# Kernel optimization log

Measured on AMD Instinct MI355X. Metric: run time of the kernel, lower is better.

Reference implementation:

```python
import jax, jax.numpy as jnp
import numpy as np

B, T, D = 2, 2048, 2048
H, DH, DR, DL = 16, 128, 64, 512
WINDOW, STRIDE, GLOBAL = 512, 64, 128
BASE, MAX_SEQ, ORIG_MAX = 10000.0, 131072, 4096
BETA_FAST, BETA_SLOW = 32.0, 1.0
SCALE = 1.0 / np.sqrt(DH)
SCALE_ROPE = 1.0 / np.sqrt(DR)


def _yarn_inv_freq():
    base_inv = 1.0 / (BASE ** (np.arange(0, DR, 2, dtype=np.float32) / DR))
    scale = MAX_SEQ / ORIG_MAX
    freqs = np.arange(DR // 2, dtype=np.float32)
    ramp = np.clip((freqs - BETA_SLOW) / (BETA_FAST - BETA_SLOW), 0.0, 1.0)
    return jnp.asarray(base_inv * (1 - ramp) + (base_inv / scale) * ramp)

_INV_FREQ = _yarn_inv_freq()
_YARN_FACTOR = np.float32(0.1 * np.log(MAX_SEQ / ORIG_MAX) + 1.0)


def _apply_rope(x):
    # x: [B, H, T, DR]
    t = jnp.arange(x.shape[2], dtype=jnp.float32)
    fr = t[:, None] * _INV_FREQ[None, :]            # [T, DR/2]
    emb = jnp.concatenate([fr, fr], axis=-1)        # [T, DR]
    cos, sin = jnp.cos(emb), jnp.sin(emb)
    x1, x2 = jnp.split(x, 2, axis=-1)
    rot = jnp.concatenate([-x2, x1], axis=-1)
    return (x * cos + rot * sin) * _YARN_FACTOR


def _sparse_mask(seq_len):
    pos = jnp.arange(seq_len)
    qp, kp = pos[:, None], pos[None, :]
    dist = qp - kp
    half = WINDOW // 2
    window = (dist >= -half) & (dist <= half)
    dilated = (kp % STRIDE == 0) | (kp < GLOBAL)
    causal = kp <= qp
    return (window | dilated) & causal              # [T, T] bool


def setup_inputs() -> dict:
    key = jax.random.key(0)
    ks = jax.random.split(key, 9)
    s = 0.02
    return {
        "x": jax.random.normal(ks[0], (B, T, D), jnp.float32),
        "w_q": jax.random.normal(ks[1], (D, D), jnp.float32) * s,
        "w_dkv": jax.random.normal(ks[2], (D, DL), jnp.float32) * s,
        "w_uk": jax.random.normal(ks[3], (DL, D), jnp.float32) * s,
        "w_uv": jax.random.normal(ks[4], (DL, D), jnp.float32) * s,
        "w_q_pos": jax.random.normal(ks[5], (D, H * DR), jnp.float32) * s,
        "w_k_pos": jax.random.normal(ks[6], (D, H * DR), jnp.float32) * s,
        "w_o": jax.random.normal(ks[7], (D, D), jnp.float32) * s,
    }


def reference(x, w_q, w_dkv, w_uk, w_uv, w_q_pos, w_k_pos, w_o):
    b, t, _ = x.shape
    # MLA projections
    q_c = (x @ w_q).reshape(b, t, H, DH).transpose(0, 2, 1, 3)      # [B,H,T,DH]
    c_kv = x @ w_dkv                                                # [B,T,DL]
    k_c = (c_kv @ w_uk).reshape(b, t, H, DH).transpose(0, 2, 1, 3)
    v_c = (c_kv @ w_uv).reshape(b, t, H, DH).transpose(0, 2, 1, 3)
    # decoupled RoPE branch (YaRN)
    q_r = (x @ w_q_pos).reshape(b, t, H, DR).transpose(0, 2, 1, 3)
    k_r = (x @ w_k_pos).reshape(b, t, H, DR).transpose(0, 2, 1, 3)
    q_r = _apply_rope(q_r)
    k_r = _apply_rope(k_r)
    # combined content + positional scores
    scores = jnp.einsum("bhqd,bhkd->bhqk", q_c, k_c) * SCALE \
           + jnp.einsum("bhqr,bhkr->bhqk", q_r, k_r) * SCALE_ROPE
    mask = _sparse_mask(t)                                          # [T,T]
    scores = jnp.where(mask[None, None], scores, -jnp.inf)
    attn = jax.nn.softmax(scores, axis=-1)
    out = jnp.einsum("bhqk,bhkd->bhqd", attn, v_c)                  # [B,H,T,DH]
    out = out.transpose(0, 2, 1, 3).reshape(b, t, D)
    return out @ w_o
```

## Files before the change

kernel.cpp:

```cpp
#include <hip/hip_runtime.h>
#include <hip/hip_bf16.h>
#include <cstdint>

typedef __attribute__((ext_vector_type(8))) short short8_t;
typedef __attribute__((ext_vector_type(4))) short short4_t;
typedef __attribute__((ext_vector_type(4))) float f32x4_t;

#define AS1 __attribute__((address_space(1)))
#define AS3 __attribute__((address_space(3)))

__device__ __forceinline__ void gload_lds16(const void* g, void* l) {
  __builtin_amdgcn_global_load_lds((const AS1 void*)g, (AS3 void*)l, 16, 0, 0);
}

__device__ __forceinline__ short8_t ld8(const __hip_bfloat16* p) {
  return *(const short8_t*)p;
}

__global__ __launch_bounds__(256) void k_prep(
    const float* __restrict__ x, __hip_bfloat16* __restrict__ xb,
    const float* __restrict__ wq,  const float* __restrict__ wqp,
    const float* __restrict__ wkp, const float* __restrict__ wdkv,
    const float* __restrict__ wuk, const float* __restrict__ wuv,
    const float* __restrict__ wo,
    __hip_bfloat16* __restrict__ Bt1, __hip_bfloat16* __restrict__ Bt2,
    __hip_bfloat16* __restrict__ woT) {
  __shared__ float t[64][65];
  int bid = blockIdx.x;
  if (bid < 4096) {
    int i = (bid * 256 + threadIdx.x) * 8;
    union { short8_t v; __hip_bfloat16 h[8]; } u;
#pragma unroll
    for (int j = 0; j < 8; ++j) u.h[j] = __float2bfloat16(x[i + j]);
    *(short8_t*)(xb + i) = u.v;
    return;
  }
  bid -= 4096;
  const float* in; __hip_bfloat16* out; int R, C, tile;
  if (bid < 1024)      { in = wq;   out = Bt1;                 R = 2048; C = 2048; tile = bid; }
  else if (bid < 1536) { in = wqp;  out = Bt1 + 2048UL * 2048; R = 2048; C = 1024; tile = bid - 1024; }
  else if (bid < 2048) { in = wkp;  out = Bt1 + 3072UL * 2048; R = 2048; C = 1024; tile = bid - 1536; }
  else if (bid < 2304) { in = wdkv; out = Bt1 + 4096UL * 2048; R = 2048; C = 512;  tile = bid - 2048; }
  else if (bid < 2560) { in = wuk;  out = Bt2;                 R = 512;  C = 2048; tile = bid - 2304; }
  else if (bid < 2816) { in = wuv;  out = Bt2 + 2048UL * 512;  R = 512;  C = 2048; tile = bid - 2560; }
  else                 { in = wo;   out = woT;                 R = 2048; C = 2048; tile = bid - 2816; }
  int nct = C >> 6;
  int ct = tile % nct, rt = tile / nct;
  int r0 = rt << 6, c0 = ct << 6;
#pragma unroll
  for (int i = 0; i < 16; ++i) {
    int idx = i * 256 + threadIdx.x;
    int r = idx >> 6, c = idx & 63;
    t[r][c] = in[(size_t)(r0 + r) * C + c0 + c];
  }
  __syncthreads();
#pragma unroll
  for (int i = 0; i < 16; ++i) {
    int idx = i * 256 + threadIdx.x;
    int c = idx >> 6, r = idx & 63;
    out[(size_t)(c0 + c) * R + r0 + r] = __float2bfloat16(t[r][c]);
  }
}

template<int MODE>
__global__ __launch_bounds__(256) void k_gemm2(const __hip_bfloat16* __restrict__ A,
                                               const __hip_bfloat16* __restrict__ Bt,
                                               int K, int nbx,
                                               void* __restrict__ O0, float alpha) {
  __shared__ __align__(16) __hip_bfloat16 Al[3][128 * 32];
  __shared__ __align__(16) __hip_bfloat16 Bl[3][128 * 32];
  int bx = blockIdx.x % nbx, by = blockIdx.x / nbx;
  int tid = threadIdx.x, lane = tid & 63, w = tid >> 6;
  int L = lane & 15, hi = lane >> 4;
  int wr = (w >> 1) << 6, wc = (w & 1) << 6;
  f32x4_t acc[4][4] = {};
  const __hip_bfloat16* Ag = A + (size_t)(by * 128) * K;
  const __hip_bfloat16* Bg = Bt + (size_t)(bx * 128) * K;
  int rA = w * 16 + (lane >> 2);
  int cA = ((lane & 3) ^ ((lane >> 3) & 3)) * 8;
  int NT = K >> 5;

  auto stage = [&](int s) {
    int j = s % 3;
    int k0 = s << 5;
    gload_lds16(Ag + (size_t)rA * K + k0 + cA,        &Al[j][(w * 16) * 32]);
    gload_lds16(Ag + (size_t)(rA + 64) * K + k0 + cA, &Al[j][(64 + w * 16) * 32]);
    gload_lds16(Bg + (size_t)rA * K + k0 + cA,        &Bl[j][(w * 16) * 32]);
    gload_lds16(Bg + (size_t)(rA + 64) * K + k0 + cA, &Bl[j][(64 + w * 16) * 32]);
  };

  stage(0); stage(1);
  asm volatile("s_waitcnt vmcnt(4)\ns_barrier" ::: "memory");

  int hs = hi ^ ((L >> 1) & 3);
  for (int t = 0; t < NT; ++t) {
    int j = t % 3;
    short8_t af[4], bf[4];
#pragma unroll
    for (int m = 0; m < 4; ++m) af[m] = ld8(&Al[j][(wr + 16 * m + L) * 32 + 8 * hs]);
#pragma unroll
    for (int n = 0; n < 4; ++n) bf[n] = ld8(&Bl[j][(wc + 16 * n + L) * 32 + 8 * hs]);
    if (t + 2 < NT) stage(t + 2);
    __builtin_amdgcn_s_setprio(1);
#pragma unroll
    for (int m = 0; m < 4; ++m)
#pragma unroll
      for (int n = 0; n < 4; ++n)
        acc[m][n] = __builtin_amdgcn_mfma_f32_16x16x32_bf16(af[m], bf[n], acc[m][n], 0, 0, 0);
    __builtin_amdgcn_s_setprio(0);
    if (t + 2 < NT)      asm volatile("s_waitcnt vmcnt(4)\ns_barrier" ::: "memory");
    else if (t + 1 < NT) asm volatile("s_waitcnt vmcnt(0)\ns_barrier" ::: "memory");
  }

  int r0 = by * 128 + wr + 4 * hi;
  int c0 = bx * 128 + wc;
  size_t N = (size_t)nbx << 7;
  float* C = (float*)O0;
#pragma unroll
  for (int m = 0; m < 4; ++m)
#pragma unroll
    for (int n = 0; n < 4; ++n)
#pragma unroll
      for (int i = 0; i < 4; ++i)
        C[(size_t)(r0 + 16 * m + i) * N + c0 + 16 * n + L] = acc[m][n][i] * alpha;
}

__global__ __launch_bounds__(256) void k_gemm_ks(const __hip_bfloat16* __restrict__ A,
                                                 const __hip_bfloat16* __restrict__ Bt,
                                                 int lda, int nbx,
                                                 float* __restrict__ P0,
                                                 float* __restrict__ P1) {
  __shared__ __align__(16) __hip_bfloat16 Al[3][128 * 32];
  __shared__ __align__(16) __hip_bfloat16 Bl[3][128 * 32];
  int part = blockIdx.x >> 7;
  int id = blockIdx.x & 127;
  int bx = id % nbx, by = id / nbx;
  int tid = threadIdx.x, lane = tid & 63, w = tid >> 6;
  int L = lane & 15, hi = lane >> 4;
  int wr = (w >> 1) << 6, wc = (w & 1) << 6;
  f32x4_t acc[4][4] = {};
  const __hip_bfloat16* Ag = A + (size_t)(by * 128) * lda + part * 1024;
  const __hip_bfloat16* Bg = Bt + (size_t)(bx * 128) * lda + part * 1024;
  int rA = w * 16 + (lane >> 2);
  int cA = ((lane & 3) ^ ((lane >> 3) & 3)) * 8;
  const int NT = 32;

  auto stage = [&](int s) {
    int j = s % 3;
    int k0 = s << 5;
    gload_lds16(Ag + (size_t)rA * lda + k0 + cA,        &Al[j][(w * 16) * 32]);
    gload_lds16(Ag + (size_t)(rA + 64) * lda + k0 + cA, &Al[j][(64 + w * 16) * 32]);
    gload_lds16(Bg + (size_t)rA * lda + k0 + cA,        &Bl[j][(w * 16) * 32]);
    gload_lds16(Bg + (size_t)(rA + 64) * lda + k0 + cA, &Bl[j][(64 + w * 16) * 32]);
  };

  stage(0); stage(1);
  asm volatile("s_waitcnt vmcnt(4)\ns_barrier" ::: "memory");

  int hs = hi ^ ((L >> 1) & 3);
  for (int t = 0; t < NT; ++t) {
    int j = t % 3;
    short8_t af[4], bf[4];
#pragma unroll
    for (int m = 0; m < 4; ++m) af[m] = ld8(&Al[j][(wr + 16 * m + L) * 32 + 8 * hs]);
#pragma unroll
    for (int n = 0; n < 4; ++n) bf[n] = ld8(&Bl[j][(wc + 16 * n + L) * 32 + 8 * hs]);
    if (t + 2 < NT) stage(t + 2);
    __builtin_amdgcn_s_setprio(1);
#pragma unroll
    for (int m = 0; m < 4; ++m)
#pragma unroll
      for (int n = 0; n < 4; ++n)
        acc[m][n] = __builtin_amdgcn_mfma_f32_16x16x32_bf16(af[m], bf[n], acc[m][n], 0, 0, 0);
    __builtin_amdgcn_s_setprio(0);
    if (t + 2 < NT)      asm volatile("s_waitcnt vmcnt(4)\ns_barrier" ::: "memory");
    else if (t + 1 < NT) asm volatile("s_waitcnt vmcnt(0)\ns_barrier" ::: "memory");
  }

  float* C = part ? P1 : P0;
  int r0 = by * 128 + wr + 4 * hi;
  int c0 = bx * 128 + wc;
#pragma unroll
  for (int m = 0; m < 4; ++m)
#pragma unroll
    for (int n = 0; n < 4; ++n)
#pragma unroll
      for (int i = 0; i < 4; ++i)
        C[(size_t)(r0 + 16 * m + i) * 512 + c0 + 16 * n + L] = acc[m][n][i];
}

__global__ __launch_bounds__(256) void k_addc(const float* __restrict__ P0,
                                              const float* __restrict__ P1,
                                              __hip_bfloat16* __restrict__ ckv) {
  int i = (blockIdx.x * 256 + threadIdx.x) * 4;
  float4 a = *(const float4*)(P0 + i);
  float4 b = *(const float4*)(P1 + i);
  union { short4_t v; __hip_bfloat16 h[4]; } u;
  u.h[0] = __float2bfloat16(a.x + b.x);
  u.h[1] = __float2bfloat16(a.y + b.y);
  u.h[2] = __float2bfloat16(a.z + b.z);
  u.h[3] = __float2bfloat16(a.w + b.w);
  *(short4_t*)(ckv + i) = u.v;
}

template<int MODE>
__global__ __launch_bounds__(512, 2) void k_gemm8(const __hip_bfloat16* __restrict__ A,
                                                  const __hip_bfloat16* __restrict__ Bt,
                                                  int K, int nbx,
                                                  void* __restrict__ O0, void* __restrict__ O1,
                                                  void* __restrict__ O2) {
  __shared__ __align__(16) __hip_bfloat16 Al[3][256 * 32];
  __shared__ __align__(16) __hip_bfloat16 Bl[3][256 * 32];
  int bx = blockIdx.x % nbx, by = blockIdx.x / nbx;
  int tid = threadIdx.x, lane = tid & 63, w = tid >> 6;
  int L = lane & 15, hi = lane >> 4;
  int wr = (w >> 2) << 7;
  int wc = (w & 3) << 6;
  f32x4_t acc[8][4] = {};
  const __hip_bfloat16* Ag = A + (size_t)(by * 256) * K;
  const __hip_bfloat16* Bg = Bt + (size_t)(bx * 256) * K;
  int rA = w * 16 + (lane >> 2);
  int cA = ((lane & 3) ^ ((lane >> 3) & 3)) * 8;
  int NT = K >> 5;

  auto stage = [&](int s) {
    int j = s % 3;
    int k0 = s << 5;
    gload_lds16(Ag + (size_t)rA * K + k0 + cA,         &Al[j][(w * 16) * 32]);
    gload_lds16(Ag + (size_t)(rA + 128) * K + k0 + cA, &Al[j][(128 + w * 16) * 32]);
    gload_lds16(Bg + (size_t)rA * K + k0 + cA,         &Bl[j][(w * 16) * 32]);
    gload_lds16(Bg + (size_t)(rA + 128) * K + k0 + cA, &Bl[j][(128 + w * 16) * 32]);
  };

  stage(0); stage(1);
  asm volatile("s_waitcnt vmcnt(4)\ns_barrier" ::: "memory");

  int hs = hi ^ ((L >> 1) & 3);
  for (int t = 0; t < NT; ++t) {
    int j = t % 3;
    short8_t af[8], bf[4];
#pragma unroll
    for (int m = 0; m < 8; ++m) af[m] = ld8(&Al[j][(wr + 16 * m + L) * 32 + 8 * hs]);
#pragma unroll
    for (int n = 0; n < 4; ++n) bf[n] = ld8(&Bl[j][(wc + 16 * n + L) * 32 + 8 * hs]);
    if (t + 2 < NT) stage(t + 2);
    __builtin_amdgcn_s_setprio(1);
#pragma unroll
    for (int m = 0; m < 8; ++m)
#pragma unroll
      for (int n = 0; n < 4; ++n)
        acc[m][n] = __builtin_amdgcn_mfma_f32_16x16x32_bf16(af[m], bf[n], acc[m][n], 0, 0, 0);
    __builtin_amdgcn_s_setprio(0);
    if (t + 2 < NT)      asm volatile("s_waitcnt vmcnt(4)\ns_barrier" ::: "memory");
    else if (t + 1 < NT) asm volatile("s_waitcnt vmcnt(0)\ns_barrier" ::: "memory");
  }

  int r0 = by * 256 + wr + 4 * hi;
  int cb = bx * 256 + wc;

  if (MODE == 2) {
    __hip_bfloat16* qcb = (__hip_bfloat16*)O0;
    __hip_bfloat16* qrb = (__hip_bfloat16*)O1;
    __hip_bfloat16* krb = (__hip_bfloat16*)O2;
    if (cb < 2048) {
      const float SCALE = 0.08838834764831845f;
#pragma unroll
      for (int m = 0; m < 8; ++m)
#pragma unroll
        for (int n = 0; n < 4; ++n)
#pragma unroll
          for (int i = 0; i < 4; ++i)
            qcb[(size_t)(r0 + 16 * m + i) * 2048 + cb + 16 * n + L] =
                __float2bfloat16(acc[m][n][i] * SCALE);
    } else {
      bool isq = cb < 3072;
      __hip_bfloat16* dst = isq ? qrb : krb;
      float osc = isq ? 0.16832169878499666f : 1.3465735902799727f;
      int cbl = cb - (isq ? 2048 : 3072);
      float invf[2];
#pragma unroll
      for (int p = 0; p < 2; ++p) {
        float fi = (float)(16 * p + L);
        float bi = __expf(fi * -0.28782313662425574f);
        float ramp = fminf(fmaxf((fi - 1.0f) * (1.0f / 31.0f), 0.0f), 1.0f);
        invf[p] = bi * (1.0f - ramp * (31.0f / 32.0f));
      }
#pragma unroll
      for (int m = 0; m < 8; ++m)
#pragma unroll
        for (int i = 0; i < 4; ++i) {
          int row = r0 + 16 * m + i;
          float ft = (float)(row & 2047);
#pragma unroll
          for (int p = 0; p < 2; ++p) {
            float sn, cs;
            __sincosf(ft * invf[p], &sn, &cs);
            float x1 = acc[m][p][i], x2 = acc[m][p + 2][i];
            dst[(size_t)row * 1024 + cbl + 16 * p + L] =
                __float2bfloat16((x1 * cs - x2 * sn) * osc);
            dst[(size_t)row * 1024 + cbl + 32 + 16 * p + L] =
                __float2bfloat16((x2 * cs + x1 * sn) * osc);
          }
        }
    }
  } else if (MODE == 3) {
    __hip_bfloat16* kcb = (__hip_bfloat16*)O0;
    __hip_bfloat16* vcb = (__hip_bfloat16*)O1;
    __hip_bfloat16* vT  = (__hip_bfloat16*)O2;
    if (cb < 2048) {
#pragma unroll
      for (int m = 0; m < 8; ++m)
#pragma unroll
        for (int n = 0; n < 4; ++n)
#pragma unroll
          for (int i = 0; i < 4; ++i)
            kcb[(size_t)(r0 + 16 * m + i) * 2048 + cb + 16 * n + L] =
                __float2bfloat16(acc[m][n][i]);
    } else {
#pragma unroll
      for (int m = 0; m < 8; ++m)
#pragma unroll
        for (int n = 0; n < 4; ++n) {
          int vcol = cb - 2048 + 16 * n + L;
          int hh = vcol >> 7, dh = vcol & 127;
          int row0 = r0 + 16 * m;
          int b = row0 >> 11, t0 = row0 & 2047;
          union { short4_t v; __hip_bfloat16 h4[4]; } pk;
#pragma unroll
          for (int i = 0; i < 4; ++i) {
            __hip_bfloat16 bv = __float2bfloat16(acc[m][n][i]);
            vcb[(size_t)(row0 + i) * 2048 + vcol] = bv;
            pk.h4[i] = bv;
          }
          *(short4_t*)(vT + ((size_t)((b * 16 + hh) * 128 + dh) * 2048 + t0)) = pk.v;
        }
    }
  }
}

__global__ __launch_bounds__(256) void k_attn(const __hip_bfloat16* __restrict__ qc,
                                              const __hip_bfloat16* __restrict__ kc,
                                              const __hip_bfloat16* __restrict__ vcb,
                                              const __hip_bfloat16* __restrict__ qr,
                                              const __hip_bfloat16* __restrict__ kr,
                                              const __hip_bfloat16* __restrict__ vT,
                                              __hip_bfloat16* __restrict__ ao) {
  const int T = 2048;
  int bid = blockIdx.x;
  int qt = 31 - (bid >> 5);
  int bh = bid & 31;
  int b = bh >> 4, h = bh & 15;
  int tid = threadIdx.x, lane = tid & 63, w = tid >> 6;
  int L = lane & 15, hi = lane >> 4;
  int q0 = qt * 64;

  __shared__ __align__(16) __hip_bfloat16 Kl[64 * 192];
  __shared__ __align__(16) __hip_bfloat16 Vt[128 * 64];
  __shared__ __align__(16) __hip_bfloat16 Pl[4][16 * 64];
  char* Klb = (char*)Kl;
  char* Vtb = (char*)Vt;
  char* Plb = (char*)Pl;

  const __hip_bfloat16* vTb = vT + (size_t)(b * 16 + h) * 128 * 2048;

  int qrow = q0 + w * 16 + L;
  size_t qb = (size_t)b * T + qrow;
  short8_t qf[6];
#pragma unroll
  for (int c = 0; c < 4; ++c)
    qf[c] = ld8(qc + qb * 2048 + h * 128 + 32 * c + 8 * hi);
#pragma unroll
  for (int c = 0; c < 2; ++c)
    qf[4 + c] = ld8(qr + qb * 1024 + h * 64 + 32 * c + 8 * hi);

  f32x4_t oacc[8] = {};
  float lpart[4] = {0.0f, 0.0f, 0.0f, 0.0f};

  int nd = qt - 6;

  for (int step = 0; step <= qt + 1; ++step) {
    bool compact = (step == qt + 1);
    if (compact && nd <= 0) break;
    int kt = step;
    if (!compact && kt > 1 && kt < qt - 4) continue;
    int k0 = kt * 64;

#pragma unroll
    for (int i = 0; i < 6; ++i) {
      int o = i * 256 + tid;
      int rr = o / 24;
      int cs = o % 24;
      int c = cs ^ (rr & 7);
      int d = c * 8;
      int srcr = compact ? ((rr < nd) ? 64 * (2 + rr) : 0) : (k0 + rr);
      size_t krow = (size_t)b * T + srcr;
      const __hip_bfloat16* src = (d < 128)
          ? kc + krow * 2048 + h * 128 + d
          : kr + krow * 1024 + h * 64 + (d - 128);
      gload_lds16(src, Klb + (i * 256 + w * 64) * 16);
    }
    if (!compact) {
#pragma unroll
      for (int i = 0; i < 4; ++i) {
        int o = i * 256 + tid;
        int row = o >> 3, cs = o & 7;
        int c = cs ^ (row & 7);
        gload_lds16(vTb + (size_t)row * 2048 + k0 + c * 8,
                    Vtb + (i * 256 + w * 64) * 16);
      }
    } else {
#pragma unroll
      for (int i = 0; i < 2; ++i) {
        int ch = i * 256 + tid;
        int jj = ch >> 4, d0 = (ch & 15) * 8;
        if (jj < nd) {
          union { short8_t v; __hip_bfloat16 hh[8]; } u;
          u.v = ld8(vcb + (size_t)(b * 2048 + 64 * (2 + jj)) * 2048 + h * 128 + d0);
#pragma unroll
          for (int qq = 0; qq < 8; ++qq) {
            int dh = d0 + qq;
            int swc = (jj >> 3) ^ (dh & 7);
            *(__hip_bfloat16*)(Vtb + dh * 128 + 16 * swc + 2 * (jj & 7)) = u.hh[qq];
          }
        }
      }
    }
    __syncthreads();

    f32x4_t sacc[4] = {};
    __builtin_amdgcn_s_setprio(1);
#pragma unroll
    for (int n = 0; n < 4; ++n) {
      int row = 16 * n + L;
#pragma unroll
      for (int c = 0; c < 6; ++c) {
        short8_t bfr = *(const short8_t*)(Klb + row * 384 + 16 * ((4 * c + hi) ^ (row & 7)));
        sacc[n] = __builtin_amdgcn_mfma_f32_16x16x32_bf16(qf[c], bfr, sacc[n], 0, 0, 0);
      }
    }
    __builtin_amdgcn_s_setprio(0);

    int rbase = q0 + w * 16 + 4 * hi;
#pragma unroll
    for (int n = 0; n < 4; ++n) {
      int col = L + 16 * n;
      int k = k0 + col;
#pragma unroll
      for (int i = 0; i < 4; ++i) {
        int rq = rbase + i;
        bool ok = compact ? (col < nd)
                          : ((k <= rq) && ((rq - k <= 256) || ((k & 63) == 0) || (k < 128)));
        float e = ok ? __expf(sacc[n][i]) : 0.0f;
        lpart[i] += e;
        int row = 4 * hi + i;
        int cc = (2 * n + (L >> 3)) ^ (row & 7);
        *(__hip_bfloat16*)(Plb + w * 2048 + row * 128 + 16 * cc + 2 * (L & 7)) =
            __float2bfloat16(e);
      }
    }

    __builtin_amdgcn_s_setprio(1);
#pragma unroll
    for (int ks = 0; ks < 2; ++ks) {
      short8_t pa = *(const short8_t*)(Plb + w * 2048 + L * 128 +
                                       16 * ((4 * ks + hi) ^ (L & 7)));
#pragma unroll
      for (int n = 0; n < 8; ++n) {
        int vrow = 16 * n + L;
        int chunk = (4 * ks + hi) ^ (vrow & 7);
        short8_t bv = *(const short8_t*)(Vtb + vrow * 128 + 16 * chunk);
        oacc[n] = __builtin_amdgcn_mfma_f32_16x16x32_bf16(pa, bv, oacc[n], 0, 0, 0);
      }
    }
    __builtin_amdgcn_s_setprio(0);
    __syncthreads();
  }

  for (int d = 1; d < 16; d <<= 1)
#pragma unroll
    for (int i = 0; i < 4; ++i) lpart[i] += __shfl_xor(lpart[i], d, 64);

#pragma unroll
  for (int n = 0; n < 8; ++n)
#pragma unroll
    for (int i = 0; i < 4; ++i) {
      int rq = q0 + w * 16 + 4 * hi + i;
      int cdh = 16 * n + L;
      float v = oacc[n][i] / lpart[i];
      ao[((size_t)b * T + rq) * 2048 + h * 128 + cdh] = __float2bfloat16(v);
    }
}

extern "C" void kernel_launch(void* const* d_in, const int* in_sizes, int n_in,
                              void* d_out, int out_size, void* d_ws, size_t ws_size,
                              hipStream_t stream) {
  const float* x     = (const float*)d_in[0];
  const float* w_q   = (const float*)d_in[1];
  const float* w_dkv = (const float*)d_in[2];
  const float* w_uk  = (const float*)d_in[3];
  const float* w_uv  = (const float*)d_in[4];
  const float* w_qp  = (const float*)d_in[5];
  const float* w_kp  = (const float*)d_in[6];
  const float* w_o   = (const float*)d_in[7];
  float* out = (float*)d_out;

  char* ws = (char*)d_ws;
  size_t off = 0;
  auto alloc = [&](size_t elems) {
    __hip_bfloat16* p = (__hip_bfloat16*)(ws + off);
    off += ((elems * 2 + 255) & ~(size_t)255);
    return p;
  };
  __hip_bfloat16* xb  = alloc(8388608);
  __hip_bfloat16* Bt1 = alloc(4608UL * 2048);
  __hip_bfloat16* Bt2 = alloc(4096UL * 512);
  __hip_bfloat16* woT = alloc(4194304);
  __hip_bfloat16* qcb = alloc(8388608);
  __hip_bfloat16* ckv = alloc(2097152);
  __hip_bfloat16* kcb = alloc(8388608);
  __hip_bfloat16* vcb = alloc(8388608);
  __hip_bfloat16* qrb = alloc(4194304);
  __hip_bfloat16* krb = alloc(4194304);
  __hip_bfloat16* aob = alloc(8388608);
  __hip_bfloat16* vT  = alloc(8388608);

  float* P0 = (float*)aob;
  float* P1 = P0 + 2097152;

  k_prep<<<7936, 256, 0, stream>>>(x, xb, w_q, w_qp, w_kp, w_dkv, w_uk, w_uv, w_o,
                                   Bt1, Bt2, woT);

  k_gemm_ks<<<256, 256, 0, stream>>>(xb, Bt1 + 4096UL * 2048, 2048, 4, P0, P1);
  k_addc<<<2048, 256, 0, stream>>>(P0, P1, ckv);

  k_gemm8<2><<<16 * 16, 512, 0, stream>>>(xb, Bt1, 2048, 16, qcb, qrb, krb);
  k_gemm8<3><<<16 * 16, 512, 0, stream>>>(ckv, Bt2, 512, 16, kcb, vcb, vT);

  k_attn<<<1024, 256, 0, stream>>>(qcb, kcb, vcb, qrb, krb, vT, aob);

  k_gemm2<1><<<16 * 32, 256, 0, stream>>>(aob, woT, 2048, 16, out, 1.0f);
}
```

Baseline: 244.8 us.

## Switch gemm to double-buffered BK=64 tiles with XOR-swizzled LDS layout

Replaces the 3-stage, BK=32 LDS pipeline in the bf16 GEMM with a 2-stage pipeline using BK=64 tiles. Each tile now goes through an 8-way XOR swizzle on 16-byte chunks. It halves the number of barriers and K-loop iterations and widens each global-to-LDS load batch. In exchange it prefetches only one tile ahead, waits on vmcnt(0) every iteration, and uses more LDS: 128 KB instead of 96 KB, which may limit the two blocks per CU that the launch bounds ask for.

```diff
diff --git a/kernel.cpp b/kernel.cpp
--- a/kernel.cpp
+++ b/kernel.cpp
@@ -209,8 +209,8 @@
                                                   int K, int nbx,
                                                   void* __restrict__ O0, void* __restrict__ O1,
                                                   void* __restrict__ O2) {
-  __shared__ __align__(16) __hip_bfloat16 Al[3][256 * 32];
-  __shared__ __align__(16) __hip_bfloat16 Bl[3][256 * 32];
+  __shared__ __align__(16) __hip_bfloat16 Al[2][256 * 64];
+  __shared__ __align__(16) __hip_bfloat16 Bl[2][256 * 64];
   int bx = blockIdx.x % nbx, by = blockIdx.x / nbx;
   int tid = threadIdx.x, lane = tid & 63, w = tid >> 6;
   int L = lane & 15, hi = lane >> 4;
@@ -219,40 +219,55 @@
   f32x4_t acc[8][4] = {};
   const __hip_bfloat16* Ag = A + (size_t)(by * 256) * K;
   const __hip_bfloat16* Bg = Bt + (size_t)(bx * 256) * K;
-  int rA = w * 16 + (lane >> 2);
-  int cA = ((lane & 3) ^ ((lane >> 3) & 3)) * 8;
-  int NT = K >> 5;
+  int NT = K >> 6;
 
   auto stage = [&](int s) {
-    int j = s % 3;
-    int k0 = s << 5;
-    gload_lds16(Ag + (size_t)rA * K + k0 + cA,         &Al[j][(w * 16) * 32]);
-    gload_lds16(Ag + (size_t)(rA + 128) * K + k0 + cA, &Al[j][(128 + w * 16) * 32]);
-    gload_lds16(Bg + (size_t)rA * K + k0 + cA,         &Bl[j][(w * 16) * 32]);
-    gload_lds16(Bg + (size_t)(rA + 128) * K + k0 + cA, &Bl[j][(128 + w * 16) * 32]);
+    int j = s & 1;
+    int k0 = s << 6;
+#pragma unroll
+    for (int i = 0; i < 4; ++i) {
+      int o = i * 512 + tid;
+      int rr = o >> 3, cs = o & 7;
+      int c = cs ^ (rr & 7);
+      gload_lds16(Ag + (size_t)rr * K + k0 + c * 8, (char*)Al[j] + (size_t)o * 16);
+    }
+#pragma unroll
+    for (int i = 0; i < 4; ++i) {
+      int o = i * 512 + tid;
+      int rr = o >> 3, cs = o & 7;
+      int c = cs ^ (rr & 7);
+      gload_lds16(Bg + (size_t)rr * K + k0 + c * 8, (char*)Bl[j] + (size_t)o * 16);
+    }
   };
 
-  stage(0); stage(1);
-  asm volatile("s_waitcnt vmcnt(4)\ns_barrier" ::: "memory");
-
-  int hs = hi ^ ((L >> 1) & 3);
+  stage(0);
+  asm volatile("s_waitcnt vmcnt(0)\ns_barrier" ::: "memory");
+
   for (int t = 0; t < NT; ++t) {
-    int j = t % 3;
-    short8_t af[8], bf[4];
-#pragma unroll
-    for (int m = 0; m < 8; ++m) af[m] = ld8(&Al[j][(wr + 16 * m + L) * 32 + 8 * hs]);
-#pragma unroll
-    for (int n = 0; n < 4; ++n) bf[n] = ld8(&Bl[j][(wc + 16 * n + L) * 32 + 8 * hs]);
-    if (t + 2 < NT) stage(t + 2);
-    __builtin_amdgcn_s_setprio(1);
-#pragma unroll
-    for (int m = 0; m < 8; ++m)
-#pragma unroll
-      for (int n = 0; n < 4; ++n)
-        acc[m][n] = __builtin_amdgcn_mfma_f32_16x16x32_bf16(af[m], bf[n], acc[m][n], 0, 0, 0);
-    __builtin_amdgcn_s_setprio(0);
-    if (t + 2 < NT)      asm volatile("s_waitcnt vmcnt(4)\ns_barrier" ::: "memory");
-    else if (t + 1 < NT) asm volatile("s_waitcnt vmcnt(0)\ns_barrier" ::: "memory");
+    int j = t & 1;
+    if (t + 1 < NT) stage(t + 1);
+#pragma unroll
+    for (int sub = 0; sub < 2; ++sub) {
+      short8_t af[8], bf[4];
+#pragma unroll
+      for (int m = 0; m < 8; ++m) {
+        int row = wr + 16 * m + L;
+        af[m] = *(const short8_t*)((char*)Al[j] + row * 128 + 16 * ((4 * sub + hi) ^ (row & 7)));
+      }
+#pragma unroll
+      for (int n = 0; n < 4; ++n) {
+        int row = wc + 16 * n + L;
+        bf[n] = *(const short8_t*)((char*)Bl[j] + row * 128 + 16 * ((4 * sub + hi) ^ (row & 7)));
+      }
+      __builtin_amdgcn_s_setprio(1);
+#pragma unroll
+      for (int m = 0; m < 8; ++m)
+#pragma unroll
+        for (int n = 0; n < 4; ++n)
+          acc[m][n] = __builtin_amdgcn_mfma_f32_16x16x32_bf16(af[m], bf[n], acc[m][n], 0, 0, 0);
+      __builtin_amdgcn_s_setprio(0);
+    }
+    if (t + 1 < NT) asm volatile("s_waitcnt vmcnt(0)\ns_barrier" ::: "memory");
   }
 
   int r0 = by * 256 + wr + 4 * hi;
```

Result: slower. 251.5 us (+2.8%).

## Double-buffer K tiles in sparse attention and precompute visited key-tile list

Applied to the files above, without the earlier changes.

The attention kernel now double-buffers the K/RoPE-K shared-memory tile, so the next tile's global-to-LDS loads are issued before the current tile's QK MFMAs. The skipped-tile loop becomes an explicit list of key-tile offsets. __syncthreads is replaced by hand-placed s_waitcnt vmcnt/lgkmcnt plus s_barrier. V staging is still single-buffered and is loaded after the PV step, and the compact-path V load is now unconditional with a clamped row index. This aims to hide K-load latency, at the cost of more LDS and fragile manual wait counts that must match the number of outstanding loads.

```diff
diff --git a/kernel.cpp b/kernel.cpp
--- a/kernel.cpp
+++ b/kernel.cpp
@@ -354,10 +354,9 @@
   int L = lane & 15, hi = lane >> 4;
   int q0 = qt * 64;
 
-  __shared__ __align__(16) __hip_bfloat16 Kl[64 * 192];
+  __shared__ __align__(16) __hip_bfloat16 Kl[2][64 * 192];
   __shared__ __align__(16) __hip_bfloat16 Vt[128 * 64];
   __shared__ __align__(16) __hip_bfloat16 Pl[4][16 * 64];
-  char* Klb = (char*)Kl;
   char* Vtb = (char*)Vt;
   char* Plb = (char*)Pl;
 
@@ -378,28 +377,37 @@
 
   int nd = qt - 6;
 
-  for (int step = 0; step <= qt + 1; ++step) {
-    bool compact = (step == qt + 1);
-    if (compact && nd <= 0) break;
-    int kt = step;
-    if (!compact && kt > 1 && kt < qt - 4) continue;
-    int k0 = kt * 64;
-
+  int k0s[9]; int ns = 0;
+  if (qt <= 6) {
+    for (int s = 0; s <= qt; ++s) k0s[ns++] = s * 64;
+  } else {
+    k0s[ns++] = 0; k0s[ns++] = 64;
+    for (int s = qt - 4; s <= qt; ++s) k0s[ns++] = s * 64;
+    if (nd > 0) k0s[ns++] = -1;
+  }
+
+  auto stageK = [&](int idx, int jbuf) {
+    bool cp = (k0s[idx] < 0);
+    int k0 = cp ? 0 : k0s[idx];
+    char* Kb = (char*)Kl[jbuf];
 #pragma unroll
     for (int i = 0; i < 6; ++i) {
       int o = i * 256 + tid;
-      int rr = o / 24;
-      int cs = o % 24;
+      int rr = o / 24, cs = o % 24;
       int c = cs ^ (rr & 7);
       int d = c * 8;
-      int srcr = compact ? ((rr < nd) ? 64 * (2 + rr) : 0) : (k0 + rr);
+      int srcr = cp ? ((rr < nd) ? 64 * (2 + rr) : 0) : (k0 + rr);
       size_t krow = (size_t)b * T + srcr;
       const __hip_bfloat16* src = (d < 128)
           ? kc + krow * 2048 + h * 128 + d
           : kr + krow * 1024 + h * 64 + (d - 128);
-      gload_lds16(src, Klb + (i * 256 + w * 64) * 16);
-    }
-    if (!compact) {
+      gload_lds16(src, Kb + (i * 256 + w * 64) * 16);
+    }
+  };
+  auto stageV = [&](int idx) {
+    bool cp = (k0s[idx] < 0);
+    if (!cp) {
+      int k0 = k0s[idx];
 #pragma unroll
       for (int i = 0; i < 4; ++i) {
         int o = i * 256 + tid;
@@ -413,9 +421,10 @@
       for (int i = 0; i < 2; ++i) {
         int ch = i * 256 + tid;
         int jj = ch >> 4, d0 = (ch & 15) * 8;
+        int jc = (jj < nd) ? jj : (nd - 1);
+        union { short8_t v; __hip_bfloat16 hh[8]; } u;
+        u.v = ld8(vcb + (size_t)(b * 2048 + 64 * (2 + jc)) * 2048 + h * 128 + d0);
         if (jj < nd) {
-          union { short8_t v; __hip_bfloat16 hh[8]; } u;
-          u.v = ld8(vcb + (size_t)(b * 2048 + 64 * (2 + jj)) * 2048 + h * 128 + d0);
 #pragma unroll
           for (int qq = 0; qq < 8; ++qq) {
             int dh = d0 + qq;
@@ -425,8 +434,21 @@
         }
       }
     }
-    __syncthreads();
-
+  };
+
+  stageK(0, 0);
+  stageV(0);
+  asm volatile("s_waitcnt vmcnt(4)\ns_barrier" ::: "memory");
+
+  int buf = 0;
+  for (int t = 0; t < ns; ++t) {
+    bool compact = (k0s[t] < 0);
+    int k0 = compact ? 0 : k0s[t];
+    bool hasNext = (t + 1 < ns);
+
+    if (hasNext) stageK(t + 1, buf ^ 1);
+
+    char* Klb = (char*)Kl[buf];
     f32x4_t sacc[4] = {};
     __builtin_amdgcn_s_setprio(1);
 #pragma unroll
@@ -459,6 +481,9 @@
       }
     }
 
+    if (hasNext) asm volatile("s_waitcnt vmcnt(6) lgkmcnt(0)\ns_barrier" ::: "memory");
+    else         asm volatile("s_waitcnt vmcnt(0) lgkmcnt(0)\ns_barrier" ::: "memory");
+
     __builtin_amdgcn_s_setprio(1);
 #pragma unroll
     for (int ks = 0; ks < 2; ++ks) {
@@ -473,7 +498,14 @@
       }
     }
     __builtin_amdgcn_s_setprio(0);
-    __syncthreads();
+
+    if (hasNext) {
+      asm volatile("s_barrier" ::: "memory");
+      stageV(t + 1);
+      if (k0s[t + 1] < 0) asm volatile("s_waitcnt vmcnt(2)\ns_barrier" ::: "memory");
+      else                asm volatile("s_waitcnt vmcnt(4)\ns_barrier" ::: "memory");
+      buf ^= 1;
+    }
   }
 
   for (int d = 1; d < 16; d <<= 1)
```

New measurement: 246.8 us. No clear change (+0.8%).
